# Performance work log

Hardware: AMD Instinct MI355X
Metric: run time of the kernel (lower is better)

The kernel has to match this reference:

```python
import jax, jax.numpy as jnp
import numpy as np

DIM = 128
K = 256
WIDTH = 0.125
POWER = 16.0
MIN_STEP = 1e-4
MAX_STEP = 0.9999
MASK_VALUE = -1e30


def setup_inputs() -> dict:
    key = jax.random.key(0)
    k1, k2, k3, k4 = jax.random.split(key, 4)
    B, L, D = 16, 4096, DIM
    s1 = 1.0 / np.sqrt(D)
    s2 = 1.0 / np.sqrt(2 * D)
    return {
        "input_seq": jax.random.normal(k1, (B, L, D), dtype=jnp.float32),
        "mask": jnp.ones((B, L), dtype=jnp.float32),
        "W1": jax.random.uniform(k2, (D, 2 * D), minval=-s1, maxval=s1, dtype=jnp.float32),
        "b1": jnp.zeros((2 * D,), dtype=jnp.float32),
        "W2": jax.random.uniform(k3, (2 * D, K - 1), minval=-s2, maxval=s2, dtype=jnp.float32),
        "Wr": jax.random.uniform(k4, (D, 1), minval=-s1, maxval=s1, dtype=jnp.float32),
        "br": jnp.zeros((1,), dtype=jnp.float32),
    }


def reference(input_seq, mask, W1, b1, W2, Wr, br):
    B, L, D = input_seq.shape
    # ---- Cal_M: attention pooling over L to produce mu: [B, K-1] ----
    attn = jnp.tanh(input_seq @ W1 + b1) @ W2              # [B, L, K-1]
    m = mask[..., None]
    attn = m * attn + (1.0 - m) * MASK_VALUE
    attn = jax.nn.softmax(attn, axis=-2)                   # softmax over L
    h = jnp.einsum('bld,blk->bkd', input_seq, attn)        # [B, K-1, D]
    mu = h @ Wr[:, 0] + br[0]                              # [B, K-1]
    # ---- TSPStepWarp: modes via softmax-cumsum, then TSP cdf ----
    n_steps = mu.shape[1]                                  # K-1
    modes = jax.nn.softmax(
        jnp.concatenate([jnp.zeros((B, 1), mu.dtype), mu], axis=1), axis=1)
    modes = jnp.cumsum(modes, axis=1)[:, :-1]              # [B, K-1]
    modes = jnp.clip(modes, MIN_STEP, MAX_STEP)
    a = jnp.clip(modes - WIDTH / 2.0, 0.0, 1.0 - WIDTH)[..., None]  # [B,K-1,1]
    b = jnp.clip(a + WIDTH, WIDTH, 1.0)
    mm = modes[..., None]                                  # [B,K-1,1]
    x = jnp.linspace(0.0, 1.0, L, dtype=mu.dtype)[None, None, :]    # [1,1,L]
    left = (mm - a) / (b - a) * jnp.clip((x - a) / (mm - a), 0.0, 1.0) ** POWER
    right = 1.0 - (b - mm) / (b - a) * jnp.clip((b - x) / (b - mm), 0.0, 1.0) ** POWER
    cdf = jnp.where(x <= mm, left, right)                  # [B, K-1, L]
    gamma = cdf.sum(axis=1) / n_steps                      # [B, L]
    original_len = n_steps + 1                             # K
    # ---- Almtx: linear-kernel soft binning, fully broadcast ----
    gamma_scaled = gamma * (original_len - 1)              # [B, L]
    ks = jnp.arange(original_len, dtype=gamma.dtype)       # [K]
    almat = jnp.maximum(1.0 - jnp.abs(gamma_scaled[..., None] - ks), 0.0)  # [B,L,K]
    return gamma_scaled, almat
```

## Files before the change

### kernel.cpp

```cpp
#include <hip/hip_runtime.h>
#include <hip/hip_bf16.h>

#define LLEN 4096
#define BATCH 16
#define NROWS 65536
#define DDIM 128
#define JDIM 256
#define KM1 255
#define BR 64
#define TPITCH 266

typedef __attribute__((ext_vector_type(8))) _Float16 h8;
typedef __attribute__((ext_vector_type(4))) _Float16 h4;
typedef __attribute__((ext_vector_type(4))) float f4v;

__device__ __forceinline__ float clampf(float x, float lo, float hi) {
  return fminf(fmaxf(x, lo), hi);
}
__device__ __forceinline__ float tanh_fast(float x) {
  float e = __expf(2.0f * x);
  return 1.0f - 2.0f / (e + 1.0f);
}

__global__ void kW(const float* __restrict__ W1, const float* __restrict__ W2,
                   _Float16* __restrict__ W1P, _Float16* __restrict__ W2P) {
  const int T = blockIdx.x * 256 + threadIdx.x;
  if (T >= 192 * 64) return;
  const int frag = T >> 6, lane = T & 63;
  const int rr = lane & 15, g = lane >> 4;
  if (frag < 64) {
    const int jt = frag >> 2, ks = frag & 3;
    _Float16* base = W1P + (size_t)frag * 512 + lane * 8;
    #pragma unroll
    for (int i = 0; i < 8; ++i)
      base[i] = (_Float16)W1[(ks * 32 + 8 * g + i) * JDIM + jt * 16 + rr];
  } else {
    const int f2 = frag - 64;
    const int kt = f2 >> 3, ks = f2 & 7;
    const int k = kt * 16 + rr;
    _Float16* base = W2P + (size_t)f2 * 512 + lane * 8;
    #pragma unroll
    for (int i = 0; i < 8; ++i)
      base[i] = (k < KM1) ? (_Float16)W2[(ks * 32 + 8 * g + i) * KM1 + k] : (_Float16)0.0f;
  }
}

__launch_bounds__(512, 4)
__global__ void kF(const float* __restrict__ X,
                   const _Float16* __restrict__ W1P, const _Float16* __restrict__ W2P,
                   const float* __restrict__ b1, const float* __restrict__ Wr,
                   const float* __restrict__ mask,
                   float* __restrict__ partE, float* __restrict__ partR) {
  __shared__ _Float16 tS[BR * TPITCH];
  __shared__ float rS[BR];

  const int tid  = threadIdx.x;
  const int lane = tid & 63, wid = tid >> 6;
  const int rr = lane & 15, g = lane >> 4;
  const int mw = wid & 3;
  const int rw = wid >> 2;
  const int blk = blockIdx.x;
  const int b = blk >> 6;
  const int r_base = blk * BR;

  f4v acc[4][2];
  #pragma unroll
  for (int m = 0; m < 4; ++m)
    #pragma unroll
    for (int n = 0; n < 2; ++n) { acc[m][n][0]=0.f; acc[m][n][1]=0.f; acc[m][n][2]=0.f; acc[m][n][3]=0.f; }
  float rp[2] = {0.f, 0.f};

  h8 Wc[4], Wn[4];
  #pragma unroll
  for (int mf = 0; mf < 4; ++mf)
    Wc[mf] = *reinterpret_cast<const h8*>(W1P + (size_t)((mw * 4 + mf) * 4) * 512 + lane * 8);
  float4 xc[2][2], xn[2][2];
  #pragma unroll
  for (int nf = 0; nf < 2; ++nf) {
    const float* xp = X + (size_t)(r_base + rw * 32 + nf * 16 + rr) * DDIM + 8 * g;
    xc[nf][0] = *reinterpret_cast<const float4*>(xp);
    xc[nf][1] = *reinterpret_cast<const float4*>(xp + 4);
  }
  #pragma unroll
  for (int ks = 0; ks < 4; ++ks) {
    if (ks < 3) {
      #pragma unroll
      for (int mf = 0; mf < 4; ++mf)
        Wn[mf] = *reinterpret_cast<const h8*>(W1P + (size_t)((mw * 4 + mf) * 4 + ks + 1) * 512 + lane * 8);
      #pragma unroll
      for (int nf = 0; nf < 2; ++nf) {
        const float* xp = X + (size_t)(r_base + rw * 32 + nf * 16 + rr) * DDIM + (ks + 1) * 32 + 8 * g;
        xn[nf][0] = *reinterpret_cast<const float4*>(xp);
        xn[nf][1] = *reinterpret_cast<const float4*>(xp + 4);
      }
    }
    h8 Bx[2];
    #pragma unroll
    for (int nf = 0; nf < 2; ++nf) {
      const float xv[8] = {xc[nf][0].x, xc[nf][0].y, xc[nf][0].z, xc[nf][0].w,
                           xc[nf][1].x, xc[nf][1].y, xc[nf][1].z, xc[nf][1].w};
      #pragma unroll
      for (int i = 0; i < 8; ++i) Bx[nf][i] = (_Float16)xv[i];
      if (mw == 0) {
        const float4 w0 = *reinterpret_cast<const float4*>(Wr + ks * 32 + 8 * g);
        const float4 w1 = *reinterpret_cast<const float4*>(Wr + ks * 32 + 8 * g + 4);
        rp[nf] += xv[0]*w0.x + xv[1]*w0.y + xv[2]*w0.z + xv[3]*w0.w
                + xv[4]*w1.x + xv[5]*w1.y + xv[6]*w1.z + xv[7]*w1.w;
      }
    }
    #pragma unroll
    for (int mf = 0; mf < 4; ++mf)
      #pragma unroll
      for (int nf = 0; nf < 2; ++nf)
        acc[mf][nf] = __builtin_amdgcn_mfma_f32_16x16x32_f16(Wc[mf], Bx[nf], acc[mf][nf], 0, 0, 0);
    if (ks < 3) {
      #pragma unroll
      for (int mf = 0; mf < 4; ++mf) Wc[mf] = Wn[mf];
      #pragma unroll
      for (int nf = 0; nf < 2; ++nf) { xc[nf][0] = xn[nf][0]; xc[nf][1] = xn[nf][1]; }
    }
  }

  #pragma unroll
  for (int mf = 0; mf < 4; ++mf)
    Wc[mf] = *reinterpret_cast<const h8*>(W2P + (size_t)((mw * 4 + mf) * 8) * 512 + lane * 8);

  #pragma unroll
  for (int mf = 0; mf < 4; ++mf) {
    const int j0 = (mw * 4 + mf) * 16 + 4 * g;
    const float4 bv = *reinterpret_cast<const float4*>(b1 + j0);
    const float bva[4] = {bv.x, bv.y, bv.z, bv.w};
    #pragma unroll
    for (int nf = 0; nf < 2; ++nf) {
      const int rl = rw * 32 + nf * 16 + rr;
      h4 o;
      #pragma unroll
      for (int reg = 0; reg < 4; ++reg)
        o[reg] = (_Float16)tanh_fast(acc[mf][nf][reg] + bva[reg]);
      *reinterpret_cast<h4*>(&tS[rl * TPITCH + j0]) = o;
    }
  }
  if (mw == 0) {
    #pragma unroll
    for (int nf = 0; nf < 2; ++nf) {
      rp[nf] += __shfl_xor(rp[nf], 16, 64);
      rp[nf] += __shfl_xor(rp[nf], 32, 64);
    }
    if (g == 0) {
      #pragma unroll
      for (int nf = 0; nf < 2; ++nf) rS[rw * 32 + nf * 16 + rr] = rp[nf];
    }
  }
  #pragma unroll
  for (int m = 0; m < 4; ++m)
    #pragma unroll
    for (int n = 0; n < 2; ++n) { acc[m][n][0]=0.f; acc[m][n][1]=0.f; acc[m][n][2]=0.f; acc[m][n][3]=0.f; }
  __syncthreads();

  float mv[2], rv[2];
  #pragma unroll
  for (int nf = 0; nf < 2; ++nf) {
    const int rl = rw * 32 + nf * 16 + rr;
    mv[nf] = mask[r_base + rl];
    rv[nf] = rS[rl];
  }

  #pragma unroll
  for (int ks = 0; ks < 8; ++ks) {
    if (ks < 7) {
      #pragma unroll
      for (int mf = 0; mf < 4; ++mf)
        Wn[mf] = *reinterpret_cast<const h8*>(W2P + (size_t)((mw * 4 + mf) * 8 + ks + 1) * 512 + lane * 8);
    }
    h8 Bt[2];
    #pragma unroll
    for (int nf = 0; nf < 2; ++nf) {
      const int rl = rw * 32 + nf * 16 + rr;
      Bt[nf] = *reinterpret_cast<const h8*>(&tS[rl * TPITCH + ks * 32 + 8 * g]);
    }
    #pragma unroll
    for (int mf = 0; mf < 4; ++mf)
      #pragma unroll
      for (int nf = 0; nf < 2; ++nf)
        acc[mf][nf] = __builtin_amdgcn_mfma_f32_16x16x32_f16(Wc[mf], Bt[nf], acc[mf][nf], 0, 0, 0);
    if (ks < 7) {
      #pragma unroll
      for (int mf = 0; mf < 4; ++mf) Wc[mf] = Wn[mf];
    }
  }

  float sE[4][4], sR[4][4];
  #pragma unroll
  for (int mf = 0; mf < 4; ++mf)
    #pragma unroll
    for (int reg = 0; reg < 4; ++reg) { sE[mf][reg] = 0.f; sR[mf][reg] = 0.f; }
  #pragma unroll
  for (int nf = 0; nf < 2; ++nf) {
    const float addm = (1.0f - mv[nf]) * (-1e30f);
    #pragma unroll
    for (int mf = 0; mf < 4; ++mf)
      #pragma unroll
      for (int reg = 0; reg < 4; ++reg) {
        const float e = __expf(mv[nf] * acc[mf][nf][reg] + addm);
        sE[mf][reg] += e;
        sR[mf][reg] += e * rv[nf];
      }
  }
  #pragma unroll
  for (int off = 1; off < 16; off <<= 1)
    #pragma unroll
    for (int mf = 0; mf < 4; ++mf)
      #pragma unroll
      for (int reg = 0; reg < 4; ++reg) {
        sE[mf][reg] += __shfl_xor(sE[mf][reg], off, 64);
        sR[mf][reg] += __shfl_xor(sR[mf][reg], off, 64);
      }
  if (rr == 0) {
    const int s = (blk & 63) * 2 + rw;
    float* pE = partE + (size_t)s * 4096 + b * 256;
    float* pR = partR + (size_t)s * 4096 + b * 256;
    #pragma unroll
    for (int mf = 0; mf < 4; ++mf)
      #pragma unroll
      for (int reg = 0; reg < 4; ++reg) {
        const int k = (mw * 4 + mf) * 16 + 4 * g + reg;
        pE[k] = sE[mf][reg];
        pR[k] = sR[mf][reg];
      }
  }
}

__global__ void kC(const float* __restrict__ partE, const float* __restrict__ partR,
                   const float* __restrict__ br, float* __restrict__ params) {
  __shared__ float red[256];
  __shared__ float sm[256];
  const int b = blockIdx.x;
  const int k = threadIdx.x;
  float v = 0.0f;
  if (k > 0) {
    const size_t idx = (size_t)b * 256 + (k - 1);
    float esum = 0.0f, rsum = 0.0f;
    #pragma unroll
    for (int s0 = 0; s0 < 128; s0 += 16) {
      float te[16], tr[16];
      #pragma unroll
      for (int i = 0; i < 16; ++i) te[i] = partE[(size_t)(s0 + i) * 4096 + idx];
      #pragma unroll
      for (int i = 0; i < 16; ++i) tr[i] = partR[(size_t)(s0 + i) * 4096 + idx];
      float e = 0.0f, r = 0.0f;
      #pragma unroll
      for (int i = 0; i < 16; ++i) { e += te[i]; r += tr[i]; }
      esum += e; rsum += r;
    }
    v = rsum / esum + br[0];
  }
  red[k] = v; __syncthreads();
  #pragma unroll
  for (int off = 128; off > 0; off >>= 1) {
    if (k < off) red[k] = fmaxf(red[k], red[k + off]);
    __syncthreads();
  }
  const float vmax = red[0];
  __syncthreads();
  const float e = expf(v - vmax);
  red[k] = e; __syncthreads();
  #pragma unroll
  for (int off = 128; off > 0; off >>= 1) {
    if (k < off) red[k] += red[k + off];
    __syncthreads();
  }
  const float tot = red[0];
  __syncthreads();
  sm[k] = e / tot; __syncthreads();
  for (int off = 1; off < 256; off <<= 1) {
    const float add = (k >= off) ? sm[k - off] : 0.0f;
    __syncthreads();
    sm[k] += add;
    __syncthreads();
  }
  if (k < KM1) {
    const float m  = clampf(sm[k], 1e-4f, 0.9999f);
    const float a  = clampf(m - 0.0625f, 0.0f, 0.875f);
    const float bb = clampf(a + 0.125f, 0.125f, 1.0f);
    const float ba = bb - a, ma = m - a, bm = bb - m;
    float* p = params + ((size_t)b * KM1 + k) * 8;
    *reinterpret_cast<float4*>(p)     = make_float4(m, a, bb, ma / ba);
    *reinterpret_cast<float4*>(p + 4) = make_float4(1.0f / ma, bm / ba, 1.0f / bm, 0.0f);
  }
}

__launch_bounds__(256)
__global__ void kD(const float* __restrict__ params, float* __restrict__ gamma,
                   float* __restrict__ almat) {
  __shared__ float P[KM1][8];
  __shared__ float gl[128];
  __shared__ float ph[128];
  const int lc = blockIdx.x, b = blockIdx.y;
  const int tid = threadIdx.x;
  if (tid < KM1) {
    const float* p = params + ((size_t)b * KM1 + tid) * 8;
    *reinterpret_cast<float4*>(&P[tid][0]) = *reinterpret_cast<const float4*>(p);
    *reinterpret_cast<float4*>(&P[tid][4]) = *reinterpret_cast<const float4*>(p + 4);
  }
  __syncthreads();
  const int li = tid & 127, half = tid >> 7;
  const int l = lc * 128 + li;
  const float x = (float)l * (1.0f / 4095.0f);
  float gacc = 0.0f;
  const int k0 = half * 128, k1 = half ? KM1 : 128;
  for (int k = k0; k < k1; ++k) {
    const float m = P[k][0], a = P[k][1], bb = P[k][2], cL = P[k][3];
    const float iMA = P[k][4], cR = P[k][5], iBM = P[k][6];
    float u = clampf((x - a) * iMA, 0.0f, 1.0f);
    u = u * u; u = u * u; u = u * u; u = u * u;
    float w = clampf((bb - x) * iBM, 0.0f, 1.0f);
    w = w * w; w = w * w; w = w * w; w = w * w;
    const float left  = cL * u;
    const float right = 1.0f - cR * w;
    gacc += (x <= m) ? left : right;
  }
  if (half == 0) gl[li] = gacc; else ph[li] = gacc;
  __syncthreads();
  if (tid < 128) {
    const float tot = gl[tid] + ph[tid];
    gl[tid] = tot;
    gamma[(size_t)b * LLEN + lc * 128 + tid] = tot;
  }
  __syncthreads();
  const int kg = (tid & 63) * 4;
  const int i0 = tid >> 6;
  const float kg0 = (float)kg;
  const size_t base = ((size_t)b * LLEN + (size_t)lc * 128) * 256;
  for (int s = 0; s < 32; ++s) {
    const int i = s * 4 + i0;
    const float gv = gl[i];
    float4 v;
    v.x = fmaxf(1.0f - fabsf(gv - kg0), 0.0f);
    v.y = fmaxf(1.0f - fabsf(gv - (kg0 + 1.0f)), 0.0f);
    v.z = fmaxf(1.0f - fabsf(gv - (kg0 + 2.0f)), 0.0f);
    v.w = fmaxf(1.0f - fabsf(gv - (kg0 + 3.0f)), 0.0f);
    *reinterpret_cast<float4*>(&almat[base + (size_t)i * 256 + kg]) = v;
  }
}

extern "C" void kernel_launch(void* const* d_in, const int* in_sizes, int n_in,
                              void* d_out, int out_size, void* d_ws, size_t ws_size,
                              hipStream_t stream) {
  const float* X    = (const float*)d_in[0];
  const float* mask = (const float*)d_in[1];
  const float* W1   = (const float*)d_in[2];
  const float* b1   = (const float*)d_in[3];
  const float* W2   = (const float*)d_in[4];
  const float* Wr   = (const float*)d_in[5];
  const float* br   = (const float*)d_in[6];
  float* out   = (float*)d_out;
  float* gamma = out;
  float* almat = out + NROWS;
  float* partE = almat;
  float* partR = almat + (size_t)128 * 4096;
  float* params = (float*)d_ws;
  _Float16* W1P = (_Float16*)(params + (size_t)BATCH * KM1 * 8);
  _Float16* W2P = W1P + 64 * 512;

  kW<<<48, 256, 0, stream>>>(W1, W2, W1P, W2P);
  kF<<<NROWS / BR, 512, 0, stream>>>(X, W1P, W2P, b1, Wr, mask, partE, partR);
  kC<<<BATCH, 256, 0, stream>>>(partE, partR, br, params);
  kD<<<dim3(32, BATCH), 256, 0, stream>>>(params, gamma, almat);
}
```

Baseline: 84.11 us.

## Pre-convert X to fp16 MFMA fragment layout in a prep kernel

A new prep kernel (merged with the weight packing kernel) converts the fp32 input sequence into fp16 fragments laid out in MFMA operand order and stores them in scratch space inside the output buffer. The main kernel then loads all X fragments up front as contiguous h8 vectors, and the W2 prefetch is deepened to two stages. The intent is to halve the X bytes the main kernel reads, coalesce its loads and drop the in-loop conversions. The cost is an extra full read and write pass over X in the prep kernel. The Wr projection now uses fp16-rounded X, which slightly changes precision.

```diff
diff --git a/kernel.cpp b/kernel.cpp
--- a/kernel.cpp
+++ b/kernel.cpp
@@ -22,9 +22,29 @@
   return 1.0f - 2.0f / (e + 1.0f);
 }
 
-__global__ void kW(const float* __restrict__ W1, const float* __restrict__ W2,
-                   _Float16* __restrict__ W1P, _Float16* __restrict__ W2P) {
-  const int T = blockIdx.x * 256 + threadIdx.x;
+__global__ void kP(const float* __restrict__ X,
+                   const float* __restrict__ W1, const float* __restrict__ W2,
+                   _Float16* __restrict__ W1P, _Float16* __restrict__ W2P,
+                   _Float16* __restrict__ Xf) {
+  const int blk = blockIdx.x;
+  const int tid = threadIdx.x;
+  if (blk < 1024) {
+    #pragma unroll
+    for (int c = 0; c < 4; ++c) {
+      const int chunk = blk * 1024 + c * 256 + tid;
+      const int lane = chunk & 63, ks = (chunk >> 6) & 3, rt = chunk >> 8;
+      const int rr = lane & 15, g = lane >> 4;
+      const float* xp = X + (size_t)(rt * 16 + rr) * DDIM + ks * 32 + 8 * g;
+      const float4 a = *reinterpret_cast<const float4*>(xp);
+      const float4 b2 = *reinterpret_cast<const float4*>(xp + 4);
+      h8 o;
+      o[0]=(_Float16)a.x;  o[1]=(_Float16)a.y;  o[2]=(_Float16)a.z;  o[3]=(_Float16)a.w;
+      o[4]=(_Float16)b2.x; o[5]=(_Float16)b2.y; o[6]=(_Float16)b2.z; o[7]=(_Float16)b2.w;
+      *reinterpret_cast<h8*>(Xf + (size_t)chunk * 8) = o;
+    }
+    return;
+  }
+  const int T = (blk - 1024) * 256 + tid;
   if (T >= 192 * 64) return;
   const int frag = T >> 6, lane = T & 63;
   const int rr = lane & 15, g = lane >> 4;
@@ -46,7 +66,7 @@
 }
 
 __launch_bounds__(512, 4)
-__global__ void kF(const float* __restrict__ X,
+__global__ void kF(const _Float16* __restrict__ Xf,
                    const _Float16* __restrict__ W1P, const _Float16* __restrict__ W2P,
                    const float* __restrict__ b1, const float* __restrict__ Wr,
                    const float* __restrict__ mask,
@@ -70,60 +90,52 @@
     for (int n = 0; n < 2; ++n) { acc[m][n][0]=0.f; acc[m][n][1]=0.f; acc[m][n][2]=0.f; acc[m][n][3]=0.f; }
   float rp[2] = {0.f, 0.f};
 
+  h8 xf[4][2];
+  #pragma unroll
+  for (int ks = 0; ks < 4; ++ks)
+    #pragma unroll
+    for (int nf = 0; nf < 2; ++nf) {
+      const int rt = blk * 4 + rw * 2 + nf;
+      xf[ks][nf] = *reinterpret_cast<const h8*>(Xf + ((size_t)(rt * 4 + ks) * 64 + lane) * 8);
+    }
+
   h8 Wc[4], Wn[4];
   #pragma unroll
   for (int mf = 0; mf < 4; ++mf)
     Wc[mf] = *reinterpret_cast<const h8*>(W1P + (size_t)((mw * 4 + mf) * 4) * 512 + lane * 8);
-  float4 xc[2][2], xn[2][2];
-  #pragma unroll
-  for (int nf = 0; nf < 2; ++nf) {
-    const float* xp = X + (size_t)(r_base + rw * 32 + nf * 16 + rr) * DDIM + 8 * g;
-    xc[nf][0] = *reinterpret_cast<const float4*>(xp);
-    xc[nf][1] = *reinterpret_cast<const float4*>(xp + 4);
-  }
   #pragma unroll
   for (int ks = 0; ks < 4; ++ks) {
     if (ks < 3) {
       #pragma unroll
       for (int mf = 0; mf < 4; ++mf)
         Wn[mf] = *reinterpret_cast<const h8*>(W1P + (size_t)((mw * 4 + mf) * 4 + ks + 1) * 512 + lane * 8);
-      #pragma unroll
-      for (int nf = 0; nf < 2; ++nf) {
-        const float* xp = X + (size_t)(r_base + rw * 32 + nf * 16 + rr) * DDIM + (ks + 1) * 32 + 8 * g;
-        xn[nf][0] = *reinterpret_cast<const float4*>(xp);
-        xn[nf][1] = *reinterpret_cast<const float4*>(xp + 4);
-      }
-    }
-    h8 Bx[2];
-    #pragma unroll
-    for (int nf = 0; nf < 2; ++nf) {
-      const float xv[8] = {xc[nf][0].x, xc[nf][0].y, xc[nf][0].z, xc[nf][0].w,
-                           xc[nf][1].x, xc[nf][1].y, xc[nf][1].z, xc[nf][1].w};
-      #pragma unroll
-      for (int i = 0; i < 8; ++i) Bx[nf][i] = (_Float16)xv[i];
-      if (mw == 0) {
-        const float4 w0 = *reinterpret_cast<const float4*>(Wr + ks * 32 + 8 * g);
-        const float4 w1 = *reinterpret_cast<const float4*>(Wr + ks * 32 + 8 * g + 4);
-        rp[nf] += xv[0]*w0.x + xv[1]*w0.y + xv[2]*w0.z + xv[3]*w0.w
-                + xv[4]*w1.x + xv[5]*w1.y + xv[6]*w1.z + xv[7]*w1.w;
-      }
-    }
-    #pragma unroll
-    for (int mf = 0; mf < 4; ++mf)
+    }
+    if (mw == 0) {
+      const float4 w0 = *reinterpret_cast<const float4*>(Wr + ks * 32 + 8 * g);
+      const float4 w1 = *reinterpret_cast<const float4*>(Wr + ks * 32 + 8 * g + 4);
+      const float wr[8] = {w0.x, w0.y, w0.z, w0.w, w1.x, w1.y, w1.z, w1.w};
       #pragma unroll
       for (int nf = 0; nf < 2; ++nf)
-        acc[mf][nf] = __builtin_amdgcn_mfma_f32_16x16x32_f16(Wc[mf], Bx[nf], acc[mf][nf], 0, 0, 0);
+        #pragma unroll
+        for (int i = 0; i < 8; ++i)
+          rp[nf] += (float)xf[ks][nf][i] * wr[i];
+    }
+    #pragma unroll
+    for (int mf = 0; mf < 4; ++mf)
+      #pragma unroll
+      for (int nf = 0; nf < 2; ++nf)
+        acc[mf][nf] = __builtin_amdgcn_mfma_f32_16x16x32_f16(Wc[mf], xf[ks][nf], acc[mf][nf], 0, 0, 0);
     if (ks < 3) {
       #pragma unroll
       for (int mf = 0; mf < 4; ++mf) Wc[mf] = Wn[mf];
-      #pragma unroll
-      for (int nf = 0; nf < 2; ++nf) { xc[nf][0] = xn[nf][0]; xc[nf][1] = xn[nf][1]; }
-    }
-  }
-
-  #pragma unroll
-  for (int mf = 0; mf < 4; ++mf)
+    }
+  }
+
+  #pragma unroll
+  for (int mf = 0; mf < 4; ++mf) {
     Wc[mf] = *reinterpret_cast<const h8*>(W2P + (size_t)((mw * 4 + mf) * 8) * 512 + lane * 8);
+    Wn[mf] = *reinterpret_cast<const h8*>(W2P + (size_t)((mw * 4 + mf) * 8 + 1) * 512 + lane * 8);
+  }
 
   #pragma unroll
   for (int mf = 0; mf < 4; ++mf) {
@@ -167,10 +179,11 @@
 
   #pragma unroll
   for (int ks = 0; ks < 8; ++ks) {
-    if (ks < 7) {
+    h8 Wn2[4];
+    if (ks < 6) {
       #pragma unroll
       for (int mf = 0; mf < 4; ++mf)
-        Wn[mf] = *reinterpret_cast<const h8*>(W2P + (size_t)((mw * 4 + mf) * 8 + ks + 1) * 512 + lane * 8);
+        Wn2[mf] = *reinterpret_cast<const h8*>(W2P + (size_t)((mw * 4 + mf) * 8 + ks + 2) * 512 + lane * 8);
     }
     h8 Bt[2];
     #pragma unroll
@@ -183,9 +196,11 @@
       #pragma unroll
       for (int nf = 0; nf < 2; ++nf)
         acc[mf][nf] = __builtin_amdgcn_mfma_f32_16x16x32_f16(Wc[mf], Bt[nf], acc[mf][nf], 0, 0, 0);
-    if (ks < 7) {
-      #pragma unroll
-      for (int mf = 0; mf < 4; ++mf) Wc[mf] = Wn[mf];
+    #pragma unroll
+    for (int mf = 0; mf < 4; ++mf) Wc[mf] = Wn[mf];
+    if (ks < 6) {
+      #pragma unroll
+      for (int mf = 0; mf < 4; ++mf) Wn[mf] = Wn2[mf];
     }
   }
 
@@ -358,12 +373,13 @@
   float* almat = out + NROWS;
   float* partE = almat;
   float* partR = almat + (size_t)128 * 4096;
+  _Float16* Xf = (_Float16*)(almat + (size_t)2 * 1024 * 1024);
   float* params = (float*)d_ws;
   _Float16* W1P = (_Float16*)(params + (size_t)BATCH * KM1 * 8);
   _Float16* W2P = W1P + 64 * 512;
 
-  kW<<<48, 256, 0, stream>>>(W1, W2, W1P, W2P);
-  kF<<<NROWS / BR, 512, 0, stream>>>(X, W1P, W2P, b1, Wr, mask, partE, partR);
+  kP<<<1072, 256, 0, stream>>>(X, W1, W2, W1P, W2P, Xf);
+  kF<<<NROWS / BR, 512, 0, stream>>>(Xf, W1P, W2P, b1, Wr, mask, partE, partR);
   kC<<<BATCH, 256, 0, stream>>>(partE, partR, br, params);
   kD<<<dim3(32, BATCH), 256, 0, stream>>>(params, gamma, almat);
 }
```

After: 85.29 us. About the same (+1.4%).
